# Performance work log

Measured on AMD Instinct MI355X. Metric: run time of the kernel, lower is better.

Reference implementation:

```python
import jax, jax.numpy as jnp
import numpy as np

TOP_N = 10
N_HEADS = 8

def _layernorm(x, g, b, eps=1e-5):
    mu = jnp.mean(x, axis=-1, keepdims=True)
    var = jnp.mean((x - mu) ** 2, axis=-1, keepdims=True)
    return (x - mu) * jax.lax.rsqrt(var + eps) * g + b

def setup_inputs() -> dict:
    key = jax.random.key(0)
    ks = jax.random.split(key, 16)
    B, N, D = 4096, 32768, 512
    s = 1.0 / np.sqrt(D)
    inp = {
        "visit_rep": jax.random.normal(ks[0], (B, D), jnp.float32),
        "E_mem_patient_rep": jax.random.normal(ks[1], (N, D), jnp.float32),
        "E_mem_med_rep": jax.random.normal(ks[2], (N, D), jnp.float32),
        "Wq": jax.random.uniform(ks[3], (D, D), jnp.float32, -s, s),
        "Wk": jax.random.uniform(ks[4], (D, D), jnp.float32, -s, s),
        "Wv": jax.random.uniform(ks[5], (D, D), jnp.float32, -s, s),
        "bq": jnp.zeros((D,), jnp.float32),
        "bk": jnp.zeros((D,), jnp.float32),
        "bv": jnp.zeros((D,), jnp.float32),
        "Wo": jax.random.uniform(ks[6], (D, D), jnp.float32, -s, s),
        "bo": jnp.zeros((D,), jnp.float32),
        "W1": jax.random.uniform(ks[7], (D, D), jnp.float32, -s, s),
        "b1": jax.random.uniform(ks[8], (D,), jnp.float32, -s, s),
        "W2": jax.random.uniform(ks[9], (D, D), jnp.float32, -s, s),
        "b2": jax.random.uniform(ks[10], (D,), jnp.float32, -s, s),
        "ln1_g": jnp.ones((D,), jnp.float32),
        "ln1_b": jnp.zeros((D,), jnp.float32),
        "ln2_g": jnp.ones((D,), jnp.float32),
        "ln2_b": jnp.zeros((D,), jnp.float32),
    }
    return inp

def reference(visit_rep, E_mem_patient_rep, E_mem_med_rep,
              Wq, bq, Wk, bk, Wv, bv, Wo, bo,
              W1, b1, W2, b2, ln1_g, ln1_b, ln2_g, ln2_b):
    B, D = visit_rep.shape
    H = N_HEADS
    hd = D // H
    # --- exact L2 kNN (faiss GpuIndexFlatL2 equivalent), detached ---
    q = jax.lax.stop_gradient(visit_rep)
    M = jax.lax.stop_gradient(E_mem_patient_rep)
    d2 = (jnp.sum(q * q, axis=1, keepdims=True)
          - 2.0 * q @ M.T
          + jnp.sum(M * M, axis=1)[None, :])          # [B, N]
    _, I = jax.lax.top_k(-d2, TOP_N)                    # [B, top_n]
    k = E_mem_patient_rep[I]                            # [B, top_n, D]
    v = E_mem_med_rep[I]                                # [B, top_n, D]
    # --- multihead attention, query seq-len 1 ---
    qh = (visit_rep @ Wq.T + bq).reshape(B, H, hd)
    kh = (k @ Wk.T + bk).reshape(B, TOP_N, H, hd)
    vh = (v @ Wv.T + bv).reshape(B, TOP_N, H, hd)
    scores = jnp.einsum("bhd,bnhd->bhn", qh, kh) / np.sqrt(hd)
    attn = jax.nn.softmax(scores, axis=-1)
    ctx = jnp.einsum("bhn,bnhd->bhd", attn, vh).reshape(B, D)
    attn_out = ctx @ Wo.T + bo
    # --- residual + norms + FFN (dropout = identity in eval) ---
    x = _layernorm(visit_rep + attn_out, ln1_g, ln1_b)
    ff = (jax.nn.leaky_relu(x @ W1.T + b1, 0.01)) @ W2.T + b2
    x = _layernorm(x + ff, ln2_g, ln2_b)
    return x
```

## Files before the change

### kernel.cpp

```cpp
#include <hip/hip_runtime.h>
#include <math.h>

#define BQ 4096
#define NMEM 32768
#define DD 512
#define TOPN 10
#define NBX 128
#define ENT 2048
#define NCF 16
#define LK 6
#define FINF 3.402823466e+38f
#define IMAX 0x7fffffff

typedef __attribute__((ext_vector_type(8))) short    bf16x8;
typedef __attribute__((ext_vector_type(4))) float    f32x4;
typedef __attribute__((ext_vector_type(4))) int      i32x4;

__device__ __forceinline__ unsigned short f2bf(float x) {
    unsigned int u = __float_as_uint(x);
    u += 0x7fffu + ((u >> 16) & 1u);
    return (unsigned short)(u >> 16);
}
__device__ __forceinline__ void async_copy16(const void* gp, void* lp) {
    __builtin_amdgcn_global_load_lds(
        (const __attribute__((address_space(1))) void*)gp,
        (__attribute__((address_space(3))) void*)lp, 16, 0, 0);
}
__device__ __forceinline__ bool lt_si(float s, int j, float s2, int j2) {
    return (s < s2) || (s == s2 && j < j2);
}
template<int KN>
__device__ __forceinline__ void topk_insert(float (&ts)[KN], int (&ti)[KN], float s, int j) {
    if (!lt_si(s, j, ts[KN-1], ti[KN-1])) return;
    #pragma unroll
    for (int p = KN-1; p > 0; --p) {
        if (lt_si(s, j, ts[p-1], ti[p-1])) { ts[p] = ts[p-1]; ti[p] = ti[p-1]; }
        else { ts[p] = s; ti[p] = j; return; }
    }
    ts[0] = s; ti[0] = j;
}

struct CastDesc {
    const float* in[7];
    unsigned short* out[7];
    int start[8];
};
__global__ __launch_bounds__(256) void cast_multi_kernel(CastDesc d) {
    int blk = blockIdx.x;
    int seg = 0;
    #pragma unroll
    for (int s = 0; s < 6; ++s) seg += (blk >= d.start[s + 1]) ? 1 : 0;
    int local = blk - d.start[seg];
    int i = (local * 256 + threadIdx.x) * 4;
    float4 v = *(const float4*)(d.in[seg] + i);
    ushort4 o;
    o.x = f2bf(v.x); o.y = f2bf(v.y); o.z = f2bf(v.z); o.w = f2bf(v.w);
    *(ushort4*)(d.out[seg] + i) = o;
}

__global__ __launch_bounds__(256) void cast_norm2_kernel(
        const float* __restrict__ inA, unsigned short* __restrict__ outA,
        const float* __restrict__ inB, unsigned short* __restrict__ outB,
        const float* __restrict__ inV,
        signed char* __restrict__ outA8, signed char* __restrict__ outV8,
        float* __restrict__ mnorm, float* __restrict__ msc,
        float* __restrict__ qsc) {
    const int pl = blockIdx.y;
    if (pl == 2 && blockIdx.x >= BQ / 4) return;
    const float* in = (pl == 0) ? inA : (pl == 1 ? inB : inV);
    int row = blockIdx.x * 4 + (threadIdx.x >> 6);
    int lane = threadIdx.x & 63;
    const float* r = in + (size_t)row * DD + lane * 8;
    float4 a = *(const float4*)r;
    float4 b = *(const float4*)(r + 4);
    if (pl < 2) {
        unsigned short* out = pl ? outB : outA;
        ushort4 oa, ob;
        oa.x = f2bf(a.x); oa.y = f2bf(a.y); oa.z = f2bf(a.z); oa.w = f2bf(a.w);
        ob.x = f2bf(b.x); ob.y = f2bf(b.y); ob.z = f2bf(b.z); ob.w = f2bf(b.w);
        unsigned short* op = out + (size_t)row * DD + lane * 8;
        *(ushort4*)op = oa; *(ushort4*)(op + 4) = ob;
    }
    if (pl != 1) {
        float ax = fmaxf(fmaxf(fmaxf(fabsf(a.x), fabsf(a.y)), fmaxf(fabsf(a.z), fabsf(a.w))),
                         fmaxf(fmaxf(fabsf(b.x), fabsf(b.y)), fmaxf(fabsf(b.z), fabsf(b.w))));
        float s = a.x*a.x + a.y*a.y + a.z*a.z + a.w*a.w
                + b.x*b.x + b.y*b.y + b.z*b.z + b.w*b.w;
        #pragma unroll
        for (int off = 32; off; off >>= 1) {
            ax = fmaxf(ax, __shfl_xor(ax, off, 64));
            if (pl == 0) s += __shfl_xor(s, off, 64);
        }
        ax = fmaxf(ax, 1e-30f);
        float inv = 127.0f / ax;
        int q[8];
        q[0] = __float2int_rn(a.x*inv); q[1] = __float2int_rn(a.y*inv);
        q[2] = __float2int_rn(a.z*inv); q[3] = __float2int_rn(a.w*inv);
        q[4] = __float2int_rn(b.x*inv); q[5] = __float2int_rn(b.y*inv);
        q[6] = __float2int_rn(b.z*inv); q[7] = __float2int_rn(b.w*inv);
        unsigned w0 = (q[0]&255) | ((q[1]&255)<<8) | ((q[2]&255)<<16) | ((unsigned)(q[3]&255)<<24);
        unsigned w1 = (q[4]&255) | ((q[5]&255)<<8) | ((q[6]&255)<<16) | ((unsigned)(q[7]&255)<<24);
        signed char* o8 = (pl == 0 ? outA8 : outV8) + (size_t)row * DD + lane * 8;
        *(uint2*)o8 = make_uint2(w0, w1);
        if (lane == 0) {
            if (pl == 0) { mnorm[row] = s; msc[row] = ax * (1.0f/127.0f); }
            else         { qsc[row] = ax * (1.0f/127.0f); }
        }
    }
}

__global__ __launch_bounds__(512, 2) void gemm_knn_kernel(
        const signed char* __restrict__ Q8,
        const signed char* __restrict__ M8,
        const float* __restrict__ mnorm, const float* __restrict__ msc,
        const float* __restrict__ qsc,
        unsigned* __restrict__ cand_part) {
    __shared__ __align__(16) union {
        struct { signed char A[4][256][64]; signed char B[4][256][64]; } g;
        unsigned S[64 * 260];
    } sh;
    __shared__ float qs[256];
    const int tid  = threadIdx.x;
    const int lane = tid & 63;
    const int wave = tid >> 6;
    const int quad = lane >> 4, c16 = lane & 15;
    const int wm = wave >> 2, wn = wave & 3;
    const int m0 = blockIdx.y * 256, n0 = blockIdx.x * 256;
    const int srow   = tid >> 2;
    const int schunk = (tid & 3) ^ ((tid >> 3) & 3);
    const signed char* ag = Q8 + (size_t)(m0 + srow) * DD + schunk * 16;
    const signed char* bg = M8 + (size_t)(n0 + srow) * DD + schunk * 16;
    const int cq = (quad ^ ((c16 >> 1) & 3)) * 16;

    i32x4 acc[8][4] = {};
    i32x4 af[4], bf[4];

    if (tid < 256) qs[tid] = qsc[m0 + tid];

#define STG_A(tt) do {                                                          \
    const int s_ = (tt) & 3;                                                    \
    async_copy16(ag + (size_t)(tt)*64,            &sh.g.A[s_][srow][(tid & 3) * 16]);      \
    async_copy16(ag + (size_t)(tt)*64 + 128*DD,   &sh.g.A[s_][128 + srow][(tid & 3) * 16]);\
} while (0)
#define STG_B(tt) do {                                                          \
    const int s_ = (tt) & 3;                                                    \
    async_copy16(bg + (size_t)(tt)*64,            &sh.g.B[s_][srow][(tid & 3) * 16]);      \
    async_copy16(bg + (size_t)(tt)*64 + 128*DD,   &sh.g.B[s_][128 + srow][(tid & 3) * 16]);\
} while (0)
#define RD_A(tt, mh) do {                                                       \
    const int s_ = (tt) & 3;                                                    \
    _Pragma("unroll")                                                           \
    for (int mt2 = 0; mt2 < 4; ++mt2)                                           \
        af[mt2] = *(const i32x4*)&sh.g.A[s_][wm*128 + ((mh)*4 + mt2)*16 + c16][cq];\
} while (0)
#define RD_B(tt) do {                                                           \
    const int s_ = (tt) & 3;                                                    \
    _Pragma("unroll")                                                           \
    for (int nt = 0; nt < 4; ++nt)                                              \
        bf[nt] = *(const i32x4*)&sh.g.B[s_][wn*64 + nt*16 + c16][cq];           \
} while (0)
#define MM(mh) do {                                                             \
    _Pragma("unroll")                                                           \
    for (int mt2 = 0; mt2 < 4; ++mt2)                                           \
        _Pragma("unroll")                                                       \
        for (int nt = 0; nt < 4; ++nt)                                          \
            acc[(mh)*4 + mt2][nt] = __builtin_amdgcn_mfma_i32_16x16x64_i8(      \
                af[mt2], bf[nt], acc[(mh)*4 + mt2][nt], 0, 0, 0);               \
} while (0)

    STG_A(0); STG_B(0); STG_A(1); STG_B(1); STG_A(2); STG_B(2);
    asm volatile("s_waitcnt vmcnt(8)" ::: "memory");
    __builtin_amdgcn_s_barrier();
    __builtin_amdgcn_sched_barrier(0);

    #pragma unroll
    for (int t = 0; t < 8; ++t) {
        RD_A(t, 0); RD_B(t);
        if (t + 3 < 8) STG_A(t + 3);
        __builtin_amdgcn_sched_barrier(0);
        __builtin_amdgcn_s_barrier();
        asm volatile("s_waitcnt lgkmcnt(0)" ::: "memory");
        __builtin_amdgcn_sched_barrier(0);
        __builtin_amdgcn_s_setprio(1);
        MM(0);
        __builtin_amdgcn_s_setprio(0);
        __builtin_amdgcn_sched_barrier(0);
        __builtin_amdgcn_s_barrier();
        RD_A(t, 1);
        if (t + 3 < 8) STG_B(t + 3);
        if (t <= 4)       asm volatile("s_waitcnt vmcnt(8)" ::: "memory");
        else if (t == 5)  asm volatile("s_waitcnt vmcnt(4)" ::: "memory");
        else if (t == 6)  asm volatile("s_waitcnt vmcnt(0)" ::: "memory");
        __builtin_amdgcn_sched_barrier(0);
        __builtin_amdgcn_s_barrier();
        asm volatile("s_waitcnt lgkmcnt(0)" ::: "memory");
        __builtin_amdgcn_sched_barrier(0);
        __builtin_amdgcn_s_setprio(1);
        MM(1);
        __builtin_amdgcn_s_setprio(0);
        __builtin_amdgcn_sched_barrier(0);
        __builtin_amdgcn_s_barrier();
    }
#undef STG_A
#undef STG_B
#undef RD_A
#undef RD_B
#undef MM

    float mn[4], ms2[4];
    #pragma unroll
    for (int nt = 0; nt < 4; ++nt) {
        int col = n0 + wn*64 + nt*16 + c16;
        mn[nt]  = mnorm[col];
        ms2[nt] = -2.0f * msc[col];
    }
    const int rrow = tid >> 1, rhalf = tid & 1;
    __syncthreads();
    #pragma unroll
    for (int p = 0; p < 4; ++p) {
        if (wn == p) {
            #pragma unroll
            for (int mt = 0; mt < 8; ++mt)
                #pragma unroll
                for (int nt = 0; nt < 4; ++nt) {
                    uint4 w;
                    #pragma unroll
                    for (int r = 0; r < 4; ++r) {
                        int arow = wm*128 + mt*16 + quad*4 + r;
                        float coef = ms2[nt] * qs[arow];
                        float s = fmaxf(fmaf(coef, (float)acc[mt][nt][r], mn[nt]), 0.f);
                        (&w.x)[r] = (__float_as_uint(s) & 0xFFFFFF80u)
                                  | (unsigned)((p & 1) * 64 + nt * 16 + c16);
                    }
                    *(uint4*)&sh.S[(nt*16 + c16) * 260 + wm*128 + mt*16 + quad*4] = w;
                }
        }
        __syncthreads();
        unsigned q4[4] = {0xFFFFFFFFu, 0xFFFFFFFFu, 0xFFFFFFFFu, 0xFFFFFFFFu};
        #pragma unroll
        for (int m = 0; m < 32; ++m) {
            unsigned nv = sh.S[(rhalf*32 + m) * 260 + rrow];
            #pragma unroll
            for (int i = 0; i < 4; ++i) {
                unsigned lo = min(q4[i], nv);
                nv = max(q4[i], nv);
                q4[i] = lo;
            }
        }
        unsigned p0 = (unsigned)__shfl_xor((int)q4[0], 1, 64);
        unsigned p1 = (unsigned)__shfl_xor((int)q4[1], 1, 64);
        unsigned p2 = (unsigned)__shfl_xor((int)q4[2], 1, 64);
        unsigned p3 = (unsigned)__shfl_xor((int)q4[3], 1, 64);
        if (rhalf == 0) {
            uint4 w4;
            w4.x = min(q4[0], p3); w4.y = min(q4[1], p2);
            w4.z = min(q4[2], p1); w4.w = min(q4[3], p0);
            *(uint4*)(cand_part + (size_t)(m0 + rrow) * ENT + blockIdx.x * 16 + p * 4) = w4;
        }
        __syncthreads();
    }
}

__global__ __launch_bounds__(256) void knn_select_kernel(
        const unsigned* __restrict__ cand_part,
        const float* __restrict__ Q, const float* __restrict__ Mm,
        const float* __restrict__ mnorm,
        int* __restrict__ knn_idx) {
    const int row = blockIdx.x;
    const int wave = threadIdx.x >> 6, lane = threadIdx.x & 63;
    __shared__ unsigned sk[64];
    __shared__ int      sc[64];
    __shared__ int      ids[NCF];
    __shared__ float    d2s[NCF];

    unsigned ks[LK]; int ti[LK];
    #pragma unroll
    for (int q = 0; q < LK; ++q) { ks[q] = 0xFFFFFFFFu; ti[q] = IMAX; }
    const uint4* p4 = (const uint4*)(cand_part + (size_t)row * ENT) + wave * 128;
    #pragma unroll
    for (int i = 0; i < 2; ++i) {
        uint4 v = p4[lane + 64 * i];
        #pragma unroll
        for (int e = 0; e < 4; ++e) {
            unsigned k = (&v.x)[e];
            int pos = wave * 512 + (lane + 64 * i) * 4 + e;
            int gcol = (pos >> 3) * 128 + (int)(k & 127u);
            bool cm[LK];
            #pragma unroll
            for (int q = 0; q < LK; ++q) cm[q] = k < ks[q];
            #pragma unroll
            for (int q = LK - 1; q > 0; --q) {
                unsigned tns = cm[q] ? k : ks[q];  int tni = cm[q] ? gcol : ti[q];
                ks[q] = cm[q-1] ? ks[q-1] : tns;
                ti[q] = cm[q-1] ? ti[q-1] : tni;
            }
            ks[0] = cm[0] ? k : ks[0];
            ti[0] = cm[0] ? gcol : ti[0];
        }
    }
    #pragma unroll
    for (int r = 0; r < NCF; ++r) {
        unsigned mk = ks[0]; int mi = ti[0];
        #pragma unroll
        for (int off = 1; off < 64; off <<= 1) {
            unsigned ok = (unsigned)__shfl_xor((int)mk, off, 64);
            int      oi = __shfl_xor(mi, off, 64);
            bool t = (ok < mk) || (ok == mk && oi < mi);
            mk = t ? ok : mk; mi = t ? oi : mi;
        }
        bool win = (ks[0] == mk) && (ti[0] == mi);
        #pragma unroll
        for (int q = 0; q < LK - 1; ++q) {
            ks[q] = win ? ks[q+1] : ks[q];
            ti[q] = win ? ti[q+1] : ti[q];
        }
        ks[LK-1] = win ? 0xFFFFFFFFu : ks[LK-1];
        ti[LK-1] = win ? IMAX : ti[LK-1];
        if (lane == r) { sk[wave * NCF + r] = mk; sc[wave * NCF + r] = mi; }
    }
    __syncthreads();
    if (wave == 0) {
        unsigned myk = sk[lane];
        int      myc = sc[lane];
        #pragma unroll
        for (int r = 0; r < NCF; ++r) {
            unsigned mk = myk; int mi = myc;
            #pragma unroll
            for (int off = 1; off < 64; off <<= 1) {
                unsigned ok = (unsigned)__shfl_xor((int)mk, off, 64);
                int      oi = __shfl_xor(mi, off, 64);
                bool t = (ok < mk) || (ok == mk && oi < mi);
                mk = t ? ok : mk; mi = t ? oi : mi;
            }
            bool win = (myk == mk) && (myc == mi);
            myk = win ? 0xFFFFFFFFu : myk;
            myc = win ? IMAX : myc;
            if (lane == r) ids[r] = mi;
        }
    }
    __syncthreads();
    float4 q0 = *(const float4*)(Q + (size_t)row * DD + lane * 8);
    float4 q1 = *(const float4*)(Q + (size_t)row * DD + lane * 8 + 4);
    for (int c = wave; c < NCF; c += 4) {
        int j = ids[c];
        const float* mr = Mm + (size_t)j * DD;
        float4 m0 = *(const float4*)(mr + lane * 8);
        float4 m1 = *(const float4*)(mr + lane * 8 + 4);
        float dot = q0.x*m0.x + q0.y*m0.y + q0.z*m0.z + q0.w*m0.w
                  + q1.x*m1.x + q1.y*m1.y + q1.z*m1.z + q1.w*m1.w;
        #pragma unroll
        for (int off = 32; off; off >>= 1) dot += __shfl_xor(dot, off, 64);
        if (lane == 0) d2s[c] = fmaf(-2.f, dot, mnorm[j]);
    }
    __syncthreads();
    if (threadIdx.x == 0) {
        float ts[TOPN]; int tj[TOPN];
        #pragma unroll
        for (int p = 0; p < TOPN; ++p) { ts[p] = FINF; tj[p] = IMAX; }
        for (int c = 0; c < NCF; ++c) topk_insert<TOPN>(ts, tj, d2s[c], ids[c]);
        #pragma unroll
        for (int p = 0; p < TOPN; ++p) knn_idx[row * TOPN + p] = tj[p];
    }
}

template<int ACT, int OUT_BF16>
__global__ __launch_bounds__(256) void gemm_bf16_nt(
        const unsigned short* __restrict__ A,
        const unsigned short* __restrict__ B,
        const float* __restrict__ bias,
        void* __restrict__ Cout, int ldc) {
    __shared__ __align__(16) unsigned short As[128 * 64];
    __shared__ __align__(16) unsigned short Bs[128 * 64];
    const int tid  = threadIdx.x;
    const int wave = tid >> 6, lane = tid & 63;
    const int quad = lane >> 4, c16 = lane & 15;
    const int m0 = blockIdx.y * 128, n0 = blockIdx.x * 128;
    const int wm0 = (wave >> 1) * 64, wn0 = (wave & 1) * 64;
    const int srow = wave * 32 + (lane >> 3);
    const int schunk = (lane & 7) ^ ((lane >> 3) & 7);
    const int xsw = c16 & 7;

    f32x4 acc[4][4] = {};

    for (int kt = 0; kt < DD; kt += 64) {
        __syncthreads();
        #pragma unroll
        for (int i = 0; i < 4; ++i) {
            const unsigned short* ga = A + (size_t)(m0 + srow + i * 8) * DD + kt + schunk * 8;
            async_copy16(ga, &As[(wave * 32 + i * 8) * 64]);
            const unsigned short* gb = B + (size_t)(n0 + srow + i * 8) * DD + kt + schunk * 8;
            async_copy16(gb, &Bs[(wave * 32 + i * 8) * 64]);
        }
        __syncthreads();
        #pragma unroll
        for (int ks = 0; ks < 64; ks += 32) {
            const int coff = (((ks >> 3) + quad) ^ xsw) << 3;
            bf16x8 af[4], bff[4];
            #pragma unroll
            for (int mt = 0; mt < 4; ++mt)
                af[mt] = *(const bf16x8*)&As[(wm0 + mt * 16 + c16) * 64 + coff];
            #pragma unroll
            for (int nt = 0; nt < 4; ++nt)
                bff[nt] = *(const bf16x8*)&Bs[(wn0 + nt * 16 + c16) * 64 + coff];
            #pragma unroll
            for (int mt = 0; mt < 4; ++mt)
                #pragma unroll
                for (int nt = 0; nt < 4; ++nt)
                    acc[mt][nt] = __builtin_amdgcn_mfma_f32_16x16x32_bf16(
                        af[mt], bff[nt], acc[mt][nt], 0, 0, 0);
        }
    }
    #pragma unroll
    for (int nt = 0; nt < 4; ++nt) {
        int ncol = n0 + wn0 + nt * 16 + c16;
        float bv = bias[ncol];
        #pragma unroll
        for (int mt = 0; mt < 4; ++mt) {
            size_t rbase = (size_t)(m0 + wm0 + mt * 16 + quad * 4) * ldc + ncol;
            #pragma unroll
            for (int r = 0; r < 4; ++r) {
                float v = acc[mt][nt][r] + bv;
                if (ACT == 1) v = v >= 0.f ? v : 0.01f * v;
                if (OUT_BF16) ((unsigned short*)Cout)[rbase + (size_t)r * ldc] = f2bf(v);
                else          ((float*)Cout)[rbase + (size_t)r * ldc] = v;
            }
        }
    }
}

struct G3 {
    const unsigned short* A[3];
    const unsigned short* B[3];
    const float* bias[3];
    void* C[3];
    int obf[3];
};
__global__ __launch_bounds__(256) void gemm3_kernel(G3 g) {
    const int yy = blockIdx.y;
    const int z = (yy >= 512) ? 2 : (yy >= 256 ? 1 : 0);
    const int my = yy - z * 256;
    __shared__ __align__(16) unsigned short As[128 * 64];
    __shared__ __align__(16) unsigned short Bs[128 * 64];
    const unsigned short* A = g.A[z];
    const unsigned short* B = g.B[z];
    const int tid  = threadIdx.x;
    const int wave = tid >> 6, lane = tid & 63;
    const int quad = lane >> 4, c16 = lane & 15;
    const int m0 = my * 128, n0 = blockIdx.x * 128;
    const int wm0 = (wave >> 1) * 64, wn0 = (wave & 1) * 64;
    const int srow = wave * 32 + (lane >> 3);
    const int schunk = (lane & 7) ^ ((lane >> 3) & 7);
    const int xsw = c16 & 7;

    f32x4 acc[4][4] = {};

    for (int kt = 0; kt < DD; kt += 64) {
        __syncthreads();
        #pragma unroll
        for (int i = 0; i < 4; ++i) {
            const unsigned short* ga = A + (size_t)(m0 + srow + i * 8) * DD + kt + schunk * 8;
            async_copy16(ga, &As[(wave * 32 + i * 8) * 64]);
            const unsigned short* gb = B + (size_t)(n0 + srow + i * 8) * DD + kt + schunk * 8;
            async_copy16(gb, &Bs[(wave * 32 + i * 8) * 64]);
        }
        __syncthreads();
        #pragma unroll
        for (int ks = 0; ks < 64; ks += 32) {
            const int coff = (((ks >> 3) + quad) ^ xsw) << 3;
            bf16x8 af[4], bff[4];
            #pragma unroll
            for (int mt = 0; mt < 4; ++mt)
                af[mt] = *(const bf16x8*)&As[(wm0 + mt * 16 + c16) * 64 + coff];
            #pragma unroll
            for (int nt = 0; nt < 4; ++nt)
                bff[nt] = *(const bf16x8*)&Bs[(wn0 + nt * 16 + c16) * 64 + coff];
            #pragma unroll
            for (int mt = 0; mt < 4; ++mt)
                #pragma unroll
                for (int nt = 0; nt < 4; ++nt)
                    acc[mt][nt] = __builtin_amdgcn_mfma_f32_16x16x32_bf16(
                        af[mt], bff[nt], acc[mt][nt], 0, 0, 0);
        }
    }
    const int obf = g.obf[z];
    #pragma unroll
    for (int nt = 0; nt < 4; ++nt) {
        int ncol = n0 + wn0 + nt * 16 + c16;
        float bv = g.bias[z][ncol];
        #pragma unroll
        for (int mt = 0; mt < 4; ++mt) {
            size_t rbase = (size_t)(m0 + wm0 + mt * 16 + quad * 4) * DD + ncol;
            #pragma unroll
            for (int r = 0; r < 4; ++r) {
                float v = acc[mt][nt][r] + bv;
                if (obf) ((unsigned short*)g.C[z])[rbase + (size_t)r * DD] = f2bf(v);
                else     ((float*)g.C[z])[rbase + (size_t)r * DD] = v;
            }
        }
    }
}

__global__ __launch_bounds__(512) void attn_kernel(
        const float* __restrict__ qh, const unsigned short* __restrict__ Kall,
        const unsigned short* __restrict__ Vall, const int* __restrict__ knn_idx,
        unsigned short* __restrict__ ctx_b) {
    const int b = blockIdx.x;
    const int h = threadIdx.x >> 6;
    const int l = threadIdx.x & 63;
    const int col = (h << 6) + l;
    int idxs[TOPN];
    #pragma unroll
    for (int n = 0; n < TOPN; ++n) idxs[n] = knn_idx[b * TOPN + n];
    const float q = qh[(size_t)b * DD + col];
    float sc[TOPN];
    #pragma unroll
    for (int n = 0; n < TOPN; ++n) {
        float p = q * __uint_as_float((unsigned)Kall[(size_t)idxs[n] * DD + col] << 16);
        #pragma unroll
        for (int off = 32; off; off >>= 1) p += __shfl_xor(p, off, 64);
        sc[n] = p * 0.125f;
    }
    float mx = sc[0];
    #pragma unroll
    for (int n = 1; n < TOPN; ++n) mx = fmaxf(mx, sc[n]);
    float se = 0.f;
    #pragma unroll
    for (int n = 0; n < TOPN; ++n) { sc[n] = expf(sc[n] - mx); se += sc[n]; }
    const float inv = 1.f / se;
    float o = 0.f;
    #pragma unroll
    for (int n = 0; n < TOPN; ++n)
        o = fmaf(sc[n] * inv,
                 __uint_as_float((unsigned)Vall[(size_t)idxs[n] * DD + col] << 16), o);
    ctx_b[(size_t)b * DD + col] = f2bf(o);
}

template<int EMIT_BF16>
__global__ __launch_bounds__(256) void add_ln_kernel(
        const float* __restrict__ X, const float* __restrict__ Y,
        const float* __restrict__ g, const float* __restrict__ be,
        float* __restrict__ out, unsigned short* __restrict__ out_b) {
    const int row = blockIdx.x;
    const int t = threadIdx.x;
    const size_t base = (size_t)row * DD;
    float v0 = X[base + t]       + Y[base + t];
    float v1 = X[base + 256 + t] + Y[base + 256 + t];
    float s = v0 + v1, sq = v0 * v0 + v1 * v1;
    #pragma unroll
    for (int off = 32; off; off >>= 1) { s += __shfl_xor(s, off, 64); sq += __shfl_xor(sq, off, 64); }
    __shared__ float rs[4], rq[4];
    const int w = t >> 6, l = t & 63;
    if (l == 0) { rs[w] = s; rq[w] = sq; }
    __syncthreads();
    float tot  = rs[0] + rs[1] + rs[2] + rs[3];
    float totq = rq[0] + rq[1] + rq[2] + rq[3];
    float mu = tot * (1.f / DD);
    float var = totq * (1.f / DD) - mu * mu;
    float rstd = rsqrtf(var + 1e-5f);
    float o0 = (v0 - mu) * rstd * g[t]       + be[t];
    float o1 = (v1 - mu) * rstd * g[256 + t] + be[256 + t];
    out[base + t] = o0;
    out[base + 256 + t] = o1;
    if (EMIT_BF16) {
        out_b[base + t] = f2bf(o0);
        out_b[base + 256 + t] = f2bf(o1);
    }
}

extern "C" void kernel_launch(void* const* d_in, const int* in_sizes, int n_in,
                              void* d_out, int out_size, void* d_ws, size_t ws_size,
                              hipStream_t stream) {
    const float* visit = (const float*)d_in[0];
    const float* Epat  = (const float*)d_in[1];
    const float* Emed  = (const float*)d_in[2];
    const float* Wq = (const float*)d_in[3];
    const float* Wk = (const float*)d_in[4];
    const float* Wv = (const float*)d_in[5];
    const float* bq = (const float*)d_in[6];
    const float* bk = (const float*)d_in[7];
    const float* bv = (const float*)d_in[8];
    const float* Wo = (const float*)d_in[9];
    const float* bo = (const float*)d_in[10];
    const float* W1 = (const float*)d_in[11];
    const float* b1 = (const float*)d_in[12];
    const float* W2 = (const float*)d_in[13];
    const float* b2 = (const float*)d_in[14];
    const float* ln1g = (const float*)d_in[15];
    const float* ln1b = (const float*)d_in[16];
    const float* ln2g = (const float*)d_in[17];
    const float* ln2b = (const float*)d_in[18];
    float* out = (float*)d_out;

    char* base = (char*)d_ws;
    const size_t MB = 1u << 20;
    float* mnorm   = (float*)(base);
    float* msc     = (float*)(base + 256*1024);
    float* qsc     = (float*)(base + 512*1024);
    int*   knn_idx = (int*)  (base + 2*MB);
    float* qh      = (float*)(base + 3*MB);
    float* attn_o  = qh;
    float* x1      = (float*)(base + 11*MB);
    float* ff      = (float*)(base + 19*MB);
    unsigned short* Qb    = (unsigned short*)(base + 27*MB);
    unsigned short* ctx_b = (unsigned short*)(base + 31*MB);
    unsigned short* x1_b  = (unsigned short*)(base + 35*MB);
    unsigned short* h1_b  = (unsigned short*)(base + 39*MB);
    unsigned short* Wq_b  = (unsigned short*)(base + 43*MB);
    unsigned short* Wk_b  = Wq_b + 262144;
    unsigned short* Wv_b  = Wk_b + 262144;
    unsigned short* Wo_b  = Wv_b + 262144;
    unsigned short* W1_b  = Wo_b + 262144;
    unsigned short* W2_b  = W1_b + 262144;
    unsigned short* Mb     = (unsigned short*)(base + 46*MB);
    unsigned short* Emed_b = (unsigned short*)(base + 78*MB);
    unsigned short* Kall = (unsigned short*)(base + 110*MB);
    unsigned short* Vall = Kall + (size_t)NMEM * DD;
    unsigned* cand_part = (unsigned*)Kall;
    signed char* M8 = (signed char*)(base + 142*MB);
    signed char* Q8 = (signed char*)(base + 158*MB);

    cast_norm2_kernel<<<dim3(NMEM / 4, 3), 256, 0, stream>>>(
        Epat, Mb, Emed, Emed_b, visit, M8, Q8, mnorm, msc, qsc);
    CastDesc cd;
    cd.in[0] = visit; cd.out[0] = Qb;
    cd.in[1] = Wq; cd.in[2] = Wk; cd.in[3] = Wv; cd.in[4] = Wo; cd.in[5] = W1; cd.in[6] = W2;
    cd.out[1] = Wq_b; cd.out[2] = Wk_b; cd.out[3] = Wv_b; cd.out[4] = Wo_b; cd.out[5] = W1_b; cd.out[6] = W2_b;
    cd.start[0] = 0; cd.start[1] = 2048;
    for (int s = 2; s <= 7; ++s) cd.start[s] = cd.start[s-1] + 256;
    cast_multi_kernel<<<cd.start[7], 256, 0, stream>>>(cd);

    gemm_knn_kernel<<<dim3(NBX, BQ / 256), 512, 0, stream>>>(Q8, M8, mnorm, msc, qsc, cand_part);
    knn_select_kernel<<<BQ, 256, 0, stream>>>(cand_part, visit, Epat, mnorm, knn_idx);

    G3 g3;
    g3.A[0] = Mb;     g3.B[0] = Wk_b; g3.bias[0] = bk; g3.C[0] = Kall; g3.obf[0] = 1;
    g3.A[1] = Emed_b; g3.B[1] = Wv_b; g3.bias[1] = bv; g3.C[1] = Vall; g3.obf[1] = 1;
    g3.A[2] = Qb;     g3.B[2] = Wq_b; g3.bias[2] = bq; g3.C[2] = qh;   g3.obf[2] = 0;
    gemm3_kernel<<<dim3(4, 544), 256, 0, stream>>>(g3);

    attn_kernel<<<BQ, 512, 0, stream>>>(qh, Kall, Vall, knn_idx, ctx_b);

    gemm_bf16_nt<0,0><<<dim3(4, BQ / 128), 256, 0, stream>>>(ctx_b, Wo_b, bo, attn_o, DD);
    add_ln_kernel<1><<<BQ, 256, 0, stream>>>(visit, attn_o, ln1g, ln1b, x1, x1_b);
    gemm_bf16_nt<1,1><<<dim3(4, BQ / 128), 256, 0, stream>>>(x1_b, W1_b, b1, h1_b, DD);
    gemm_bf16_nt<0,0><<<dim3(4, BQ / 128), 256, 0, stream>>>(h1_b, W2_b, b2, ff,   DD);
    add_ln_kernel<0><<<BQ, 256, 0, stream>>>(x1, ff, ln2g, ln2b, out, nullptr);
}
```

Before: 572.1 us.

## Shrink kNN GEMM tile to 128 rows, load A directly, raise occupancy

The int8 distance GEMM tile drops from 256x256 to 128x256. The query (A) operand is now read straight from global memory into registers instead of being staged through LDS, and the B buffer goes from four stages to two. This cuts LDS and register use so launch bounds can ask for four blocks per CU, and the per-tile top-4 reduction is rebuilt as a 4-way shuffle merge. The cost is twice as many blocks re-reading M8, uncoalesced direct global loads for A, and a shallower prefetch pipeline.

```diff
diff --git a/kernel.cpp b/kernel.cpp
--- a/kernel.cpp
+++ b/kernel.cpp
@@ -109,101 +109,76 @@
     }
 }
 
-__global__ __launch_bounds__(512, 2) void gemm_knn_kernel(
+__global__ __launch_bounds__(512, 4) void gemm_knn_kernel(
         const signed char* __restrict__ Q8,
         const signed char* __restrict__ M8,
         const float* __restrict__ mnorm, const float* __restrict__ msc,
         const float* __restrict__ qsc,
         unsigned* __restrict__ cand_part) {
     __shared__ __align__(16) union {
-        struct { signed char A[4][256][64]; signed char B[4][256][64]; } g;
-        unsigned S[64 * 260];
+        struct { signed char B[2][256][64]; } g;
+        unsigned S[64 * 133];
     } sh;
-    __shared__ float qs[256];
+    __shared__ float qs[128];
     const int tid  = threadIdx.x;
     const int lane = tid & 63;
     const int wave = tid >> 6;
     const int quad = lane >> 4, c16 = lane & 15;
     const int wm = wave >> 2, wn = wave & 3;
-    const int m0 = blockIdx.y * 256, n0 = blockIdx.x * 256;
+    const int m0 = blockIdx.y * 128, n0 = blockIdx.x * 256;
     const int srow   = tid >> 2;
     const int schunk = (tid & 3) ^ ((tid >> 3) & 3);
-    const signed char* ag = Q8 + (size_t)(m0 + srow) * DD + schunk * 16;
     const signed char* bg = M8 + (size_t)(n0 + srow) * DD + schunk * 16;
     const int cq = (quad ^ ((c16 >> 1) & 3)) * 16;
-
-    i32x4 acc[8][4] = {};
+    const signed char* agb = Q8 + (size_t)(m0 + wm * 64 + c16) * DD + quad * 16;
+
+    i32x4 acc[4][4] = {};
     i32x4 af[4], bf[4];
 
-    if (tid < 256) qs[tid] = qsc[m0 + tid];
-
-#define STG_A(tt) do {                                                          \
-    const int s_ = (tt) & 3;                                                    \
-    async_copy16(ag + (size_t)(tt)*64,            &sh.g.A[s_][srow][(tid & 3) * 16]);      \
-    async_copy16(ag + (size_t)(tt)*64 + 128*DD,   &sh.g.A[s_][128 + srow][(tid & 3) * 16]);\
-} while (0)
+    if (tid < 128) qs[tid] = qsc[m0 + tid];
+
 #define STG_B(tt) do {                                                          \
-    const int s_ = (tt) & 3;                                                    \
+    const int s_ = (tt) & 1;                                                    \
     async_copy16(bg + (size_t)(tt)*64,            &sh.g.B[s_][srow][(tid & 3) * 16]);      \
     async_copy16(bg + (size_t)(tt)*64 + 128*DD,   &sh.g.B[s_][128 + srow][(tid & 3) * 16]);\
 } while (0)
-#define RD_A(tt, mh) do {                                                       \
-    const int s_ = (tt) & 3;                                                    \
-    _Pragma("unroll")                                                           \
-    for (int mt2 = 0; mt2 < 4; ++mt2)                                           \
-        af[mt2] = *(const i32x4*)&sh.g.A[s_][wm*128 + ((mh)*4 + mt2)*16 + c16][cq];\
-} while (0)
 #define RD_B(tt) do {                                                           \
-    const int s_ = (tt) & 3;                                                    \
+    const int s_ = (tt) & 1;                                                    \
     _Pragma("unroll")                                                           \
     for (int nt = 0; nt < 4; ++nt)                                              \
         bf[nt] = *(const i32x4*)&sh.g.B[s_][wn*64 + nt*16 + c16][cq];           \
 } while (0)
-#define MM(mh) do {                                                             \
+#define MM() do {                                                               \
     _Pragma("unroll")                                                           \
-    for (int mt2 = 0; mt2 < 4; ++mt2)                                           \
+    for (int mt = 0; mt < 4; ++mt)                                              \
         _Pragma("unroll")                                                       \
         for (int nt = 0; nt < 4; ++nt)                                          \
-            acc[(mh)*4 + mt2][nt] = __builtin_amdgcn_mfma_i32_16x16x64_i8(      \
-                af[mt2], bf[nt], acc[(mh)*4 + mt2][nt], 0, 0, 0);               \
+            acc[mt][nt] = __builtin_amdgcn_mfma_i32_16x16x64_i8(                \
+                af[mt], bf[nt], acc[mt][nt], 0, 0, 0);                          \
 } while (0)
 
-    STG_A(0); STG_B(0); STG_A(1); STG_B(1); STG_A(2); STG_B(2);
-    asm volatile("s_waitcnt vmcnt(8)" ::: "memory");
-    __builtin_amdgcn_s_barrier();
-    __builtin_amdgcn_sched_barrier(0);
+    STG_B(0); STG_B(1);
 
     #pragma unroll
     for (int t = 0; t < 8; ++t) {
-        RD_A(t, 0); RD_B(t);
-        if (t + 3 < 8) STG_A(t + 3);
+        #pragma unroll
+        for (int mt = 0; mt < 4; ++mt)
+            af[mt] = *(const i32x4*)(agb + (size_t)mt * 16 * DD + t * 64);
+        if (t >= 1 && t < 7) STG_B(t + 1);
+        if (t == 0 || t == 7) asm volatile("s_waitcnt vmcnt(0)" ::: "memory");
+        else                  asm volatile("s_waitcnt vmcnt(2)" ::: "memory");
         __builtin_amdgcn_sched_barrier(0);
         __builtin_amdgcn_s_barrier();
+        RD_B(t);
         asm volatile("s_waitcnt lgkmcnt(0)" ::: "memory");
         __builtin_amdgcn_sched_barrier(0);
         __builtin_amdgcn_s_setprio(1);
-        MM(0);
+        MM();
         __builtin_amdgcn_s_setprio(0);
         __builtin_amdgcn_sched_barrier(0);
         __builtin_amdgcn_s_barrier();
-        RD_A(t, 1);
-        if (t + 3 < 8) STG_B(t + 3);
-        if (t <= 4)       asm volatile("s_waitcnt vmcnt(8)" ::: "memory");
-        else if (t == 5)  asm volatile("s_waitcnt vmcnt(4)" ::: "memory");
-        else if (t == 6)  asm volatile("s_waitcnt vmcnt(0)" ::: "memory");
-        __builtin_amdgcn_sched_barrier(0);
-        __builtin_amdgcn_s_barrier();
-        asm volatile("s_waitcnt lgkmcnt(0)" ::: "memory");
-        __builtin_amdgcn_sched_barrier(0);
-        __builtin_amdgcn_s_setprio(1);
-        MM(1);
-        __builtin_amdgcn_s_setprio(0);
-        __builtin_amdgcn_sched_barrier(0);
-        __builtin_amdgcn_s_barrier();
-    }
-#undef STG_A
+    }
 #undef STG_B
-#undef RD_A
 #undef RD_B
 #undef MM
 
@@ -214,48 +189,58 @@
         mn[nt]  = mnorm[col];
         ms2[nt] = -2.0f * msc[col];
     }
-    const int rrow = tid >> 1, rhalf = tid & 1;
+    float qsr[4][4];
+    #pragma unroll
+    for (int mt = 0; mt < 4; ++mt)
+        #pragma unroll
+        for (int r = 0; r < 4; ++r)
+            qsr[mt][r] = qs[wm*64 + mt*16 + quad*4 + r];
+    const int rrow = tid >> 2, rq = tid & 3;
     __syncthreads();
     #pragma unroll
     for (int p = 0; p < 4; ++p) {
         if (wn == p) {
             #pragma unroll
-            for (int mt = 0; mt < 8; ++mt)
+            for (int mt = 0; mt < 4; ++mt)
                 #pragma unroll
                 for (int nt = 0; nt < 4; ++nt) {
                     uint4 w;
                     #pragma unroll
                     for (int r = 0; r < 4; ++r) {
-                        int arow = wm*128 + mt*16 + quad*4 + r;
-                        float coef = ms2[nt] * qs[arow];
+                        float coef = ms2[nt] * qsr[mt][r];
                         float s = fmaxf(fmaf(coef, (float)acc[mt][nt][r], mn[nt]), 0.f);
                         (&w.x)[r] = (__float_as_uint(s) & 0xFFFFFF80u)
                                   | (unsigned)((p & 1) * 64 + nt * 16 + c16);
                     }
-                    *(uint4*)&sh.S[(nt*16 + c16) * 260 + wm*128 + mt*16 + quad*4] = w;
+                    *(uint4*)&sh.S[(nt*16 + c16) * 133 + wm*64 + mt*16 + quad*4] = w;
                 }
         }
         __syncthreads();
-        unsigned q4[4] = {0xFFFFFFFFu, 0xFFFFFFFFu, 0xFFFFFFFFu, 0xFFFFFFFFu};
-        #pragma unroll
-        for (int m = 0; m < 32; ++m) {
-            unsigned nv = sh.S[(rhalf*32 + m) * 260 + rrow];
-            #pragma unroll
-            for (int i = 0; i < 4; ++i) {
-                unsigned lo = min(q4[i], nv);
-                nv = max(q4[i], nv);
-                q4[i] = lo;
-            }
-        }
-        unsigned p0 = (unsigned)__shfl_xor((int)q4[0], 1, 64);
-        unsigned p1 = (unsigned)__shfl_xor((int)q4[1], 1, 64);
-        unsigned p2 = (unsigned)__shfl_xor((int)q4[2], 1, 64);
-        unsigned p3 = (unsigned)__shfl_xor((int)q4[3], 1, 64);
-        if (rhalf == 0) {
-            uint4 w4;
-            w4.x = min(q4[0], p3); w4.y = min(q4[1], p2);
-            w4.z = min(q4[2], p1); w4.w = min(q4[3], p0);
-            *(uint4*)(cand_part + (size_t)(m0 + rrow) * ENT + blockIdx.x * 16 + p * 4) = w4;
+        unsigned s0 = 0xFFFFFFFFu, s1 = 0xFFFFFFFFu, s2 = 0xFFFFFFFFu, s3 = 0xFFFFFFFFu;
+        #pragma unroll
+        for (int m = 0; m < 16; ++m) {
+            unsigned nv = sh.S[(rq*16 + m) * 133 + rrow];
+            unsigned lo;
+            lo = min(s0, nv); nv = max(s0, nv); s0 = lo;
+            lo = min(s1, nv); nv = max(s1, nv); s1 = lo;
+            lo = min(s2, nv); nv = max(s2, nv); s2 = lo;
+            lo = min(s3, nv); nv = max(s3, nv); s3 = lo;
+        }
+        unsigned p0 = (unsigned)__shfl_xor((int)s0, 1, 64);
+        unsigned p1 = (unsigned)__shfl_xor((int)s1, 1, 64);
+        unsigned p2 = (unsigned)__shfl_xor((int)s2, 1, 64);
+        unsigned p3 = (unsigned)__shfl_xor((int)s3, 1, 64);
+        unsigned b0 = min(s0, p3), b1 = min(s1, p2), b2 = min(s2, p1), b3 = min(s3, p0);
+        unsigned t0 = min(b0, b2), t2 = max(b0, b2), t1 = min(b1, b3), t3 = max(b1, b3);
+        s0 = min(t0, t1); s1 = max(t0, t1); s2 = min(t2, t3); s3 = max(t2, t3);
+        p0 = (unsigned)__shfl_xor((int)s0, 2, 64);
+        p1 = (unsigned)__shfl_xor((int)s1, 2, 64);
+        p2 = (unsigned)__shfl_xor((int)s2, 2, 64);
+        p3 = (unsigned)__shfl_xor((int)s3, 2, 64);
+        b0 = min(s0, p3); b1 = min(s1, p2); b2 = min(s2, p1); b3 = min(s3, p0);
+        if (rq == p) {
+            *(uint4*)(cand_part + (size_t)(m0 + rrow) * ENT + blockIdx.x * 16 + p * 4) =
+                make_uint4(b0, b1, b2, b3);
         }
         __syncthreads();
     }
@@ -629,7 +614,7 @@
     for (int s = 2; s <= 7; ++s) cd.start[s] = cd.start[s-1] + 256;
     cast_multi_kernel<<<cd.start[7], 256, 0, stream>>>(cd);
 
-    gemm_knn_kernel<<<dim3(NBX, BQ / 256), 512, 0, stream>>>(Q8, M8, mnorm, msc, qsc, cand_part);
+    gemm_knn_kernel<<<dim3(NBX, BQ / 128), 512, 0, stream>>>(Q8, M8, mnorm, msc, qsc, cand_part);
     knn_select_kernel<<<BQ, 256, 0, stream>>>(cand_part, visit, Epat, mnorm, knn_idx);
 
     G3 g3;
```

New measurement: 767.2 us. 34.1% more time.
